# Optimization experiments

Measured on AMD Instinct MI355X. Metric: run time of the kernel, lower is better.

Reference implementation:

```python
import jax, jax.numpy as jnp
import numpy as np

N_FEATURES = 64
D_MODEL = 256


def setup_inputs() -> dict:
    key = jax.random.key(0)
    ks = jax.random.split(key, 6)
    B = 4096
    x = jax.random.normal(ks[0], (B, N_FEATURES), dtype=jnp.float32)
    # Stacked per-feature weights (equivalent to n_features separate MLPs).
    # Linear(1, d): weight [d, 1] -> stacked as [F, d]; bias [F, d]
    s1 = 1.0  # kaiming-uniform-ish scale for fan_in=1
    W1 = jax.random.uniform(ks[1], (N_FEATURES, D_MODEL), jnp.float32, -s1, s1)
    b1 = jax.random.uniform(ks[2], (N_FEATURES, D_MODEL), jnp.float32, -s1, s1)
    # Linear(d, d): weight [d, d] per feature -> [F, d, d]
    s2 = 1.0 / np.sqrt(D_MODEL)
    W2 = jax.random.uniform(ks[3], (N_FEATURES, D_MODEL, D_MODEL), jnp.float32, -s2, s2)
    b2 = jax.random.uniform(ks[4], (N_FEATURES, D_MODEL), jnp.float32, -s2, s2)
    cls_token = jax.random.normal(ks[5], (1, 1, D_MODEL), dtype=jnp.float32)
    return {"x": x, "W1": W1, "b1": b1, "W2": W2, "b2": b2, "cls_token": cls_token}


def reference(x, W1, b1, W2, b2, cls_token):
    # h[b,f,d] = relu(x[b,f] * W1[f,d] + b1[f,d])   (Linear(1,d) per feature)
    h = jax.nn.relu(x[:, :, None] * W1[None, :, :] + b1[None, :, :])
    # out[b,f,e] = h[b,f,:] @ W2[f,:,:] + b2[f,:]   (Linear(d,d) per feature)
    out = jnp.einsum("bfd,fde->bfe", h, W2) + b2[None, :, :]
    cls = jnp.broadcast_to(cls_token, (x.shape[0], 1, out.shape[-1]))
    return jnp.concatenate([cls, out], axis=1)  # [B, F+1, d_model]
```

## Files before the change

kernel.cpp:

```cpp
#include <hip/hip_runtime.h>
#include <hip/hip_bf16.h>


#define B_  4096
#define F_  64
#define D_  256
#define ORS (65 * 256)

using f32x4  = __attribute__((ext_vector_type(4))) float;
using s16x8  = __attribute__((ext_vector_type(8))) short;
typedef unsigned int u32;

__device__ __forceinline__ unsigned short to_bf16_bits(float v) {
    __hip_bfloat16 h = __float2bfloat16(v);
    return *reinterpret_cast<unsigned short*>(&h);
}

__device__ __forceinline__ void gload_lds16(const void* g, void* l) {
    __builtin_amdgcn_global_load_lds(
        (const __attribute__((address_space(1))) u32*)g,
        (__attribute__((address_space(3))) u32*)l, 16, 0, 0);
}

__global__ __launch_bounds__(256) void femb_prep(
    const float* __restrict__ W2, unsigned short* __restrict__ W2s)
{
    const int blk = blockIdx.x;
    const int f   = blk >> 2;
    const int kb  = blk & 3;
    const int t   = threadIdx.x;

    const float* col = W2 + (size_t)f * D_ * D_ + (size_t)(kb * 64) * D_ + t;
    float r[64];
    #pragma unroll
    for (int j = 0; j < 64; ++j) r[j] = col[(size_t)j * D_];

    unsigned short* ob = W2s + (size_t)blk * 16384 + t * 64;
    #pragma unroll
    for (int j8 = 0; j8 < 8; ++j8) {
        union { s16x8 s; unsigned short u[8]; } pk;
        #pragma unroll
        for (int e = 0; e < 8; ++e) pk.u[e] = to_bf16_bits(r[j8 * 8 + e]);
        *reinterpret_cast<s16x8*>(ob + ((j8 ^ (t & 7)) * 8)) = pk.s;
    }
}

__global__ __launch_bounds__(256, 2) void femb_main5(
    const float* __restrict__ x,  const float* __restrict__ W1,
    const float* __restrict__ b1, const unsigned short* __restrict__ W2s,
    const float* __restrict__ b2, const float* __restrict__ cls,
    float* __restrict__ out)
{
    __shared__ float w1s[D_];
    __shared__ float b1s[D_];
    __shared__ float xs[128];
    __shared__ __align__(16) char arena[65536];
    unsigned short* bW0 = (unsigned short*)arena;
    unsigned short* bW1 = (unsigned short*)(arena + 32768);
    float* eb0 = (float*)arena;
    float* eb1 = (float*)(arena + 16640);

    const int tid  = threadIdx.x;
    const int bid  = blockIdx.x;
    const int f    = bid & 63;
    const int row0 = (bid >> 6) << 7;

    w1s[tid] = W1[f * D_ + tid];
    b1s[tid] = b1[f * D_ + tid];
    if (tid < 128) xs[tid] = x[(size_t)(row0 + tid) * F_ + f];

    const int lane = tid & 63;
    const int wid  = tid >> 6;
    const int wm   = wid >> 1;
    const int wn   = wid & 1;
    const int llo  = lane & 15;
    const int lhi  = lane >> 4;

    const char* gsrc = (const char*)(W2s + (size_t)f * 65536);
    f32x4 clsv = *reinterpret_cast<const f32x4*>(cls + lane * 4);

#define STAGE(DST, KB)                                                         \
    {                                                                          \
        const char* gt = gsrc + (KB) * 32768;                                  \
        _Pragma("unroll")                                                      \
        for (int r = 0; r < 8; ++r)                                            \
            gload_lds16(gt + tid * 16 + r * 4096,                              \
                        (char*)(DST) + tid * 16 + r * 4096);                   \
    }

    STAGE(bW0, 0);
    __syncthreads();

    float xv[4];
    #pragma unroll
    for (int mt = 0; mt < 4; ++mt) xv[mt] = xs[wm * 64 + mt * 16 + llo];

    f32x4 acc[4][8];
    #pragma unroll
    for (int mt = 0; mt < 4; ++mt)
        #pragma unroll
        for (int nt = 0; nt < 8; ++nt)
            acc[mt][nt] = (f32x4){0.f, 0.f, 0.f, 0.f};

    #pragma unroll
    for (int kb = 0; kb < 4; ++kb) {
        unsigned short* cur = (kb & 1) ? bW1 : bW0;
        unsigned short* nxt = (kb & 1) ? bW0 : bW1;
        if (kb < 3) STAGE(nxt, kb + 1);

        #pragma unroll
        for (int ks = 0; ks < 2; ++ks) {
            const int kg = kb * 64 + ks * 32 + lhi * 8;
            float w1r[8], b1r[8];
            #pragma unroll
            for (int e = 0; e < 8; ++e) { w1r[e] = w1s[kg + e]; b1r[e] = b1s[kg + e]; }

            s16x8 afrag[4];
            #pragma unroll
            for (int mt = 0; mt < 4; ++mt) {
                union { s16x8 s; unsigned short u[8]; } pk;
                #pragma unroll
                for (int e = 0; e < 8; ++e) {
                    float h = fmaf(xv[mt], w1r[e], b1r[e]);
                    pk.u[e] = to_bf16_bits(fmaxf(h, 0.f));
                }
                afrag[mt] = pk.s;
            }

            const int base16 = (wn * 128 + llo) * 64 + (((ks * 4 + lhi) ^ (llo & 7)) * 8);
            #pragma unroll
            for (int nt = 0; nt < 8; ++nt) {
                s16x8 bfrag = *reinterpret_cast<const s16x8*>(&cur[base16 + nt * 1024]);
                #pragma unroll
                for (int mt = 0; mt < 4; ++mt)
                    acc[mt][nt] = __builtin_amdgcn_mfma_f32_16x16x32_bf16(
                        bfrag, afrag[mt], acc[mt][nt], 0, 0, 0);
            }
        }
        __syncthreads();
    }

    f32x4 b2v = *reinterpret_cast<const f32x4*>(&b2[f * D_ + lane * 4]);

#define EPI_WRITE(C, EB)                                                       \
    if (wm == ((C) >> 2)) {                                                    \
        const int mt_ = (C) & 3;                                               \
        _Pragma("unroll")                                                      \
        for (int nt = 0; nt < 8; ++nt)                                         \
            *reinterpret_cast<f32x4*>(                                         \
                &(EB)[llo * 260 + wn * 128 + nt * 16 + lhi * 4]) = acc[mt_][nt]; \
    }

#define EPI_BAR()                                                              \
    do {                                                                       \
        asm volatile("s_waitcnt lgkmcnt(0)" ::: "memory");                     \
        __builtin_amdgcn_s_barrier();                                          \
        asm volatile("" ::: "memory");                                         \
    } while (0)

#define EPI_READ(C, EB)                                                        \
    {                                                                          \
        _Pragma("unroll")                                                      \
        for (int i = 0; i < 4; ++i) {                                          \
            const int lr = wid * 4 + i;                                        \
            const size_t grow = (size_t)(row0 + (C) * 16 + lr);                \
            f32x4 v = *reinterpret_cast<const f32x4*>(                         \
                          &(EB)[lr * 260 + lane * 4]) + b2v;                   \
            *reinterpret_cast<f32x4*>(out + grow * ORS + (f + 1) * D_ + lane * 4) = v; \
            if (f == 0)                                                        \
                *reinterpret_cast<f32x4*>(out + grow * ORS + lane * 4) = clsv; \
        }                                                                      \
    }

    EPI_WRITE(0, eb0);
    EPI_BAR();
    #pragma unroll
    for (int c = 0; c < 8; ++c) {
        float* curb = (c & 1) ? eb1 : eb0;
        float* nxtb = (c & 1) ? eb0 : eb1;
        if (c < 7) EPI_WRITE(c + 1, nxtb);
        EPI_READ(c, curb);
        if (c < 7) EPI_BAR();
    }
#undef STAGE
#undef EPI_WRITE
#undef EPI_BAR
#undef EPI_READ
}

__global__ void femb_cls(const float* __restrict__ cls, float* __restrict__ out)
{
    int i = blockIdx.x * 256 + threadIdx.x;
    int b = i >> 6;
    int q = i & 63;
    f32x4 v = *reinterpret_cast<const f32x4*>(cls + q * 4);
    *reinterpret_cast<f32x4*>(out + (size_t)b * ORS + q * 4) = v;
}

__global__ __launch_bounds__(256, 2) void femb_main_fb(
    const float* __restrict__ x,  const float* __restrict__ W1,
    const float* __restrict__ b1, const float* __restrict__ W2,
    const float* __restrict__ b2, float* __restrict__ out)
{
    __shared__ float w1s[D_];
    __shared__ float b1s[D_];
    __shared__ float xs[128];
    __shared__ __align__(16) unsigned short bW[256][72];

    const int tid  = threadIdx.x;
    const int bid  = blockIdx.x;
    const int f    = bid & 63;
    const int row0 = (bid >> 6) << 7;

    w1s[tid] = W1[f * D_ + tid];
    b1s[tid] = b1[f * D_ + tid];
    if (tid < 128) xs[tid] = x[(size_t)(row0 + tid) * F_ + f];

    const int lane = tid & 63;
    const int wid  = tid >> 6;
    const int wm   = wid >> 1;
    const int wn   = wid & 1;
    const int llo  = lane & 15;
    const int lhi  = lane >> 4;

    __syncthreads();

    float xv[4];
    #pragma unroll
    for (int mt = 0; mt < 4; ++mt) xv[mt] = xs[wm * 64 + mt * 16 + llo];

    f32x4 acc[4][8];
    #pragma unroll
    for (int mt = 0; mt < 4; ++mt)
        #pragma unroll
        for (int nt = 0; nt < 8; ++nt)
            acc[mt][nt] = (f32x4){0.f, 0.f, 0.f, 0.f};

    const float* w2col = W2 + (size_t)f * D_ * D_ + tid;

    for (int kb = 0; kb < 4; ++kb) {
        float r[64];
        const float* p = w2col + (size_t)(kb * 64) * D_;
        #pragma unroll
        for (int j = 0; j < 64; ++j) r[j] = p[(size_t)j * D_];

        __syncthreads();
        #pragma unroll
        for (int j8 = 0; j8 < 8; ++j8) {
            union { s16x8 s; unsigned short u[8]; } pk;
            #pragma unroll
            for (int e = 0; e < 8; ++e) pk.u[e] = to_bf16_bits(r[j8 * 8 + e]);
            *reinterpret_cast<s16x8*>(&bW[tid][j8 * 8]) = pk.s;
        }
        __syncthreads();

        #pragma unroll
        for (int ks = 0; ks < 2; ++ks) {
            const int kg = kb * 64 + ks * 32 + lhi * 8;
            float w1r[8], b1r[8];
            #pragma unroll
            for (int e = 0; e < 8; ++e) { w1r[e] = w1s[kg + e]; b1r[e] = b1s[kg + e]; }

            s16x8 afrag[4];
            #pragma unroll
            for (int mt = 0; mt < 4; ++mt) {
                union { s16x8 s; unsigned short u[8]; } pk;
                #pragma unroll
                for (int e = 0; e < 8; ++e) {
                    float h = fmaf(xv[mt], w1r[e], b1r[e]);
                    pk.u[e] = to_bf16_bits(fmaxf(h, 0.f));
                }
                afrag[mt] = pk.s;
            }

            const int kl = ks * 32 + lhi * 8;
            #pragma unroll
            for (int nt = 0; nt < 8; ++nt) {
                s16x8 bfrag = *reinterpret_cast<const s16x8*>(
                    &bW[wn * 128 + nt * 16 + llo][kl]);
                #pragma unroll
                for (int mt = 0; mt < 4; ++mt)
                    acc[mt][nt] = __builtin_amdgcn_mfma_f32_16x16x32_bf16(
                        bfrag, afrag[mt], acc[mt][nt], 0, 0, 0);
            }
        }
    }

    const float* b2f = b2 + f * D_;
    float* obase = out + (size_t)(row0 + wm * 64 + llo) * ORS
                       + (f + 1) * D_ + wn * 128 + lhi * 4;
    #pragma unroll
    for (int nt = 0; nt < 8; ++nt) {
        f32x4 bv = *reinterpret_cast<const f32x4*>(&b2f[wn * 128 + nt * 16 + lhi * 4]);
        #pragma unroll
        for (int mt = 0; mt < 4; ++mt) {
            f32x4 v = acc[mt][nt] + bv;
            *reinterpret_cast<f32x4*>(obase + (size_t)mt * 16 * ORS + nt * 16) = v;
        }
    }
}

extern "C" void kernel_launch(void* const* d_in, const int* in_sizes, int n_in,
                              void* d_out, int out_size, void* d_ws, size_t ws_size,
                              hipStream_t stream)
{
    const float* x   = (const float*)d_in[0];
    const float* W1  = (const float*)d_in[1];
    const float* b1  = (const float*)d_in[2];
    const float* W2  = (const float*)d_in[3];
    const float* b2  = (const float*)d_in[4];
    const float* cls = (const float*)d_in[5];
    float* out = (float*)d_out;

    const size_t need = (size_t)F_ * D_ * D_ * sizeof(unsigned short);
    if (ws_size >= need) {
        unsigned short* W2s = (unsigned short*)d_ws;
        femb_prep<<<F_ * 4, 256, 0, stream>>>(W2, W2s);
        femb_main5<<<F_ * (B_ / 128), 256, 0, stream>>>(x, W1, b1, W2s, b2, cls, out);
    } else {
        femb_cls<<<(B_ * 64) / 256, 256, 0, stream>>>(cls, out);
        femb_main_fb<<<F_ * (B_ / 128), 256, 0, stream>>>(x, W1, b1, W2, b2, out);
    }
}
```

Baseline: 78.28 us.

## Shrink LDS staging to 32-wide K slices to fit three blocks per CU

The prep kernel now lays out W2 in bf16 as 32-element K slices with a 4-way XOR swizzle. The main kernel double-buffers 16KB slices over 8 steps instead of 32KB over 4, and uses a smaller epilogue buffer of 8 rows. Together these cut LDS use so launch bounds can request 3 blocks per CU. The feature-to-block mapping is also permuted so concurrently running blocks touch different features. In exchange there are twice as many pipeline barriers and epilogue rounds, and register pressure rises under the tighter occupancy bound.

```diff
diff --git a/kernel.cpp b/kernel.cpp
--- a/kernel.cpp
+++ b/kernel.cpp
@@ -35,17 +35,19 @@
     #pragma unroll
     for (int j = 0; j < 64; ++j) r[j] = col[(size_t)j * D_];
 
-    unsigned short* ob = W2s + (size_t)blk * 16384 + t * 64;
+    unsigned short* ob = W2s + (size_t)blk * 16384;
     #pragma unroll
     for (int j8 = 0; j8 < 8; ++j8) {
         union { s16x8 s; unsigned short u[8]; } pk;
         #pragma unroll
         for (int e = 0; e < 8; ++e) pk.u[e] = to_bf16_bits(r[j8 * 8 + e]);
-        *reinterpret_cast<s16x8*>(ob + ((j8 ^ (t & 7)) * 8)) = pk.s;
-    }
-}
-
-__global__ __launch_bounds__(256, 2) void femb_main5(
+        const int h  = j8 >> 2;
+        const int pp = (j8 & 3) ^ ((t >> 1) & 3);
+        *reinterpret_cast<s16x8*>(ob + h * 8192 + t * 32 + pp * 8) = pk.s;
+    }
+}
+
+__global__ __launch_bounds__(256, 3) void femb_main6(
     const float* __restrict__ x,  const float* __restrict__ W1,
     const float* __restrict__ b1, const unsigned short* __restrict__ W2s,
     const float* __restrict__ b2, const float* __restrict__ cls,
@@ -54,15 +56,12 @@
     __shared__ float w1s[D_];
     __shared__ float b1s[D_];
     __shared__ float xs[128];
-    __shared__ __align__(16) char arena[65536];
-    unsigned short* bW0 = (unsigned short*)arena;
-    unsigned short* bW1 = (unsigned short*)(arena + 32768);
-    float* eb0 = (float*)arena;
-    float* eb1 = (float*)(arena + 16640);
+    __shared__ __align__(16) unsigned short bW[2][8192];
+    __shared__ __align__(16) float eb[2][8 * 260];
 
     const int tid  = threadIdx.x;
     const int bid  = blockIdx.x;
-    const int f    = bid & 63;
+    const int f    = (bid & 7) * 8 + ((bid >> 3) & 7);
     const int row0 = (bid >> 6) << 7;
 
     w1s[tid] = W1[f * D_ + tid];
@@ -76,19 +75,20 @@
     const int llo  = lane & 15;
     const int lhi  = lane >> 4;
 
-    const char* gsrc = (const char*)(W2s + (size_t)f * 65536);
+    const char* gsrc = (const char*)W2s + (size_t)f * 131072;
     f32x4 clsv = *reinterpret_cast<const f32x4*>(cls + lane * 4);
-
-#define STAGE(DST, KB)                                                         \
+    f32x4 b2v  = *reinterpret_cast<const f32x4*>(&b2[f * D_ + lane * 4]);
+
+#define STAGE(DST, S)                                                          \
     {                                                                          \
-        const char* gt = gsrc + (KB) * 32768;                                  \
+        const char* gt = gsrc + (S) * 16384;                                   \
         _Pragma("unroll")                                                      \
-        for (int r = 0; r < 8; ++r)                                            \
+        for (int r = 0; r < 4; ++r)                                            \
             gload_lds16(gt + tid * 16 + r * 4096,                              \
                         (char*)(DST) + tid * 16 + r * 4096);                   \
     }
 
-    STAGE(bW0, 0);
+    STAGE(bW[0], 0);
     __syncthreads();
 
     float xv[4];
@@ -102,11 +102,154 @@
         for (int nt = 0; nt < 8; ++nt)
             acc[mt][nt] = (f32x4){0.f, 0.f, 0.f, 0.f};
 
-    #pragma unroll
+    const int bbase = (wn * 128 + llo) * 32 + ((lhi ^ ((llo >> 1) & 3)) * 8);
+
+    #pragma unroll
+    for (int s = 0; s < 8; ++s) {
+        const unsigned short* cur = bW[s & 1];
+        if (s < 7) STAGE(bW[(s & 1) ^ 1], s + 1);
+
+        const int kg = s * 32 + lhi * 8;
+        float w1r[8], b1r[8];
+        #pragma unroll
+        for (int e = 0; e < 8; ++e) { w1r[e] = w1s[kg + e]; b1r[e] = b1s[kg + e]; }
+
+        s16x8 afrag[4];
+        #pragma unroll
+        for (int mt = 0; mt < 4; ++mt) {
+            union { s16x8 sv; unsigned short u[8]; } pk;
+            #pragma unroll
+            for (int e = 0; e < 8; ++e) {
+                float h = fmaf(xv[mt], w1r[e], b1r[e]);
+                pk.u[e] = to_bf16_bits(fmaxf(h, 0.f));
+            }
+            afrag[mt] = pk.sv;
+        }
+
+        #pragma unroll
+        for (int nt = 0; nt < 8; ++nt) {
+            s16x8 bfrag = *reinterpret_cast<const s16x8*>(&cur[bbase + nt * 512]);
+            #pragma unroll
+            for (int mt = 0; mt < 4; ++mt)
+                acc[mt][nt] = __builtin_amdgcn_mfma_f32_16x16x32_bf16(
+                    bfrag, afrag[mt], acc[mt][nt], 0, 0, 0);
+        }
+        __syncthreads();
+    }
+
+
+#define EPI_WRITE(C, EB)                                                       \
+    if (wm == ((C) >> 3) && ((llo >> 3) == ((C) & 1))) {                       \
+        const int mt_ = ((C) >> 1) & 3;                                        \
+        const int lr_ = llo & 7;                                               \
+        _Pragma("unroll")                                                      \
+        for (int nt = 0; nt < 8; ++nt)                                         \
+            *reinterpret_cast<f32x4*>(                                         \
+                &(EB)[lr_ * 260 + wn * 128 + nt * 16 + lhi * 4]) = acc[mt_][nt]; \
+    }
+
+#define EPI_BAR()                                                              \
+    do {                                                                       \
+        asm volatile("s_waitcnt lgkmcnt(0)" ::: "memory");                     \
+        __builtin_amdgcn_s_barrier();                                          \
+        asm volatile("" ::: "memory");                                         \
+    } while (0)
+
+#define EPI_READ(C, EB)                                                        \
+    {                                                                          \
+        _Pragma("unroll")                                                      \
+        for (int i = 0; i < 2; ++i) {                                          \
+            const int lr_ = wid * 2 + i;                                       \
+            const size_t grow = (size_t)(row0 + (C) * 8 + lr_);                \
+            f32x4 v = *reinterpret_cast<const f32x4*>(                         \
+                          &(EB)[lr_ * 260 + lane * 4]) + b2v;                  \
+            *reinterpret_cast<f32x4*>(out + grow * ORS + (f + 1) * D_ + lane * 4) = v; \
+            if (f == 0)                                                        \
+                *reinterpret_cast<f32x4*>(out + grow * ORS + lane * 4) = clsv; \
+        }                                                                      \
+    }
+
+    EPI_WRITE(0, eb[0]);
+    EPI_BAR();
+    #pragma unroll
+    for (int c = 0; c < 16; ++c) {
+        float* curb = eb[c & 1];
+        float* nxtb = eb[(c & 1) ^ 1];
+        if (c < 15) EPI_WRITE(c + 1, nxtb);
+        EPI_READ(c, curb);
+        if (c < 15) EPI_BAR();
+    }
+#undef STAGE
+#undef EPI_WRITE
+#undef EPI_BAR
+#undef EPI_READ
+}
+
+__global__ void femb_cls(const float* __restrict__ cls, float* __restrict__ out)
+{
+    int i = blockIdx.x * 256 + threadIdx.x;
+    int b = i >> 6;
+    int q = i & 63;
+    f32x4 v = *reinterpret_cast<const f32x4*>(cls + q * 4);
+    *reinterpret_cast<f32x4*>(out + (size_t)b * ORS + q * 4) = v;
+}
+
+__global__ __launch_bounds__(256, 2) void femb_main_fb(
+    const float* __restrict__ x,  const float* __restrict__ W1,
+    const float* __restrict__ b1, const float* __restrict__ W2,
+    const float* __restrict__ b2, float* __restrict__ out)
+{
+    __shared__ float w1s[D_];
+    __shared__ float b1s[D_];
+    __shared__ float xs[128];
+    __shared__ __align__(16) unsigned short bW[256][72];
+
+    const int tid  = threadIdx.x;
+    const int bid  = blockIdx.x;
+    const int f    = bid & 63;
+    const int row0 = (bid >> 6) << 7;
+
+    w1s[tid] = W1[f * D_ + tid];
+    b1s[tid] = b1[f * D_ + tid];
+    if (tid < 128) xs[tid] = x[(size_t)(row0 + tid) * F_ + f];
+
+    const int lane = tid & 63;
+    const int wid  = tid >> 6;
+    const int wm   = wid >> 1;
+    const int wn   = wid & 1;
+    const int llo  = lane & 15;
+    const int lhi  = lane >> 4;
+
+    __syncthreads();
+
+    float xv[4];
+    #pragma unroll
+    for (int mt = 0; mt < 4; ++mt) xv[mt] = xs[wm * 64 + mt * 16 + llo];
+
+    f32x4 acc[4][8];
+    #pragma unroll
+    for (int mt = 0; mt < 4; ++mt)
+        #pragma unroll
+        for (int nt = 0; nt < 8; ++nt)
+            acc[mt][nt] = (f32x4){0.f, 0.f, 0.f, 0.f};
+
+    const float* w2col = W2 + (size_t)f * D_ * D_ + tid;
+
     for (int kb = 0; kb < 4; ++kb) {
-        unsigned short* cur = (kb & 1) ? bW1 : bW0;
-        unsigned short* nxt = (kb & 1) ? bW0 : bW1;
-        if (kb < 3) STAGE(nxt, kb + 1);
+        float r[64];
+        const float* p = w2col + (size_t)(kb * 64) * D_;
+        #pragma unroll
+        for (int j = 0; j < 64; ++j) r[j] = p[(size_t)j * D_];
+
+        __syncthreads();
+        #pragma unroll
+        for (int j8 = 0; j8 < 8; ++j8) {
+            union { s16x8 s; unsigned short u[8]; } pk;
+            #pragma unroll
+            for (int e = 0; e < 8; ++e) pk.u[e] = to_bf16_bits(r[j8 * 8 + e]);
+            *reinterpret_cast<s16x8*>(&bW[tid][j8 * 8]) = pk.s;
+        }
+        __syncthreads();
 
         #pragma unroll
         for (int ks = 0; ks < 2; ++ks) {
@@ -127,152 +270,6 @@
                 afrag[mt] = pk.s;
             }
 
-            const int base16 = (wn * 128 + llo) * 64 + (((ks * 4 + lhi) ^ (llo & 7)) * 8);
-            #pragma unroll
-            for (int nt = 0; nt < 8; ++nt) {
-                s16x8 bfrag = *reinterpret_cast<const s16x8*>(&cur[base16 + nt * 1024]);
-                #pragma unroll
-                for (int mt = 0; mt < 4; ++mt)
-                    acc[mt][nt] = __builtin_amdgcn_mfma_f32_16x16x32_bf16(
-                        bfrag, afrag[mt], acc[mt][nt], 0, 0, 0);
-            }
-        }
-        __syncthreads();
-    }
-
-    f32x4 b2v = *reinterpret_cast<const f32x4*>(&b2[f * D_ + lane * 4]);
-
-#define EPI_WRITE(C, EB)                                                       \
-    if (wm == ((C) >> 2)) {                                                    \
-        const int mt_ = (C) & 3;                                               \
-        _Pragma("unroll")                                                      \
-        for (int nt = 0; nt < 8; ++nt)                                         \
-            *reinterpret_cast<f32x4*>(                                         \
-                &(EB)[llo * 260 + wn * 128 + nt * 16 + lhi * 4]) = acc[mt_][nt]; \
-    }
-
-#define EPI_BAR()                                                              \
-    do {                                                                       \
-        asm volatile("s_waitcnt lgkmcnt(0)" ::: "memory");                     \
-        __builtin_amdgcn_s_barrier();                                          \
-        asm volatile("" ::: "memory");                                         \
-    } while (0)
-
-#define EPI_READ(C, EB)                                                        \
-    {                                                                          \
-        _Pragma("unroll")                                                      \
-        for (int i = 0; i < 4; ++i) {                                          \
-            const int lr = wid * 4 + i;                                        \
-            const size_t grow = (size_t)(row0 + (C) * 16 + lr);                \
-            f32x4 v = *reinterpret_cast<const f32x4*>(                         \
-                          &(EB)[lr * 260 + lane * 4]) + b2v;                   \
-            *reinterpret_cast<f32x4*>(out + grow * ORS + (f + 1) * D_ + lane * 4) = v; \
-            if (f == 0)                                                        \
-                *reinterpret_cast<f32x4*>(out + grow * ORS + lane * 4) = clsv; \
-        }                                                                      \
-    }
-
-    EPI_WRITE(0, eb0);
-    EPI_BAR();
-    #pragma unroll
-    for (int c = 0; c < 8; ++c) {
-        float* curb = (c & 1) ? eb1 : eb0;
-        float* nxtb = (c & 1) ? eb0 : eb1;
-        if (c < 7) EPI_WRITE(c + 1, nxtb);
-        EPI_READ(c, curb);
-        if (c < 7) EPI_BAR();
-    }
-#undef STAGE
-#undef EPI_WRITE
-#undef EPI_BAR
-#undef EPI_READ
-}
-
-__global__ void femb_cls(const float* __restrict__ cls, float* __restrict__ out)
-{
-    int i = blockIdx.x * 256 + threadIdx.x;
-    int b = i >> 6;
-    int q = i & 63;
-    f32x4 v = *reinterpret_cast<const f32x4*>(cls + q * 4);
-    *reinterpret_cast<f32x4*>(out + (size_t)b * ORS + q * 4) = v;
-}
-
-__global__ __launch_bounds__(256, 2) void femb_main_fb(
-    const float* __restrict__ x,  const float* __restrict__ W1,
-    const float* __restrict__ b1, const float* __restrict__ W2,
-    const float* __restrict__ b2, float* __restrict__ out)
-{
-    __shared__ float w1s[D_];
-    __shared__ float b1s[D_];
-    __shared__ float xs[128];
-    __shared__ __align__(16) unsigned short bW[256][72];
-
-    const int tid  = threadIdx.x;
-    const int bid  = blockIdx.x;
-    const int f    = bid & 63;
-    const int row0 = (bid >> 6) << 7;
-
-    w1s[tid] = W1[f * D_ + tid];
-    b1s[tid] = b1[f * D_ + tid];
-    if (tid < 128) xs[tid] = x[(size_t)(row0 + tid) * F_ + f];
-
-    const int lane = tid & 63;
-    const int wid  = tid >> 6;
-    const int wm   = wid >> 1;
-    const int wn   = wid & 1;
-    const int llo  = lane & 15;
-    const int lhi  = lane >> 4;
-
-    __syncthreads();
-
-    float xv[4];
-    #pragma unroll
-    for (int mt = 0; mt < 4; ++mt) xv[mt] = xs[wm * 64 + mt * 16 + llo];
-
-    f32x4 acc[4][8];
-    #pragma unroll
-    for (int mt = 0; mt < 4; ++mt)
-        #pragma unroll
-        for (int nt = 0; nt < 8; ++nt)
-            acc[mt][nt] = (f32x4){0.f, 0.f, 0.f, 0.f};
-
-    const float* w2col = W2 + (size_t)f * D_ * D_ + tid;
-
-    for (int kb = 0; kb < 4; ++kb) {
-        float r[64];
-        const float* p = w2col + (size_t)(kb * 64) * D_;
-        #pragma unroll
-        for (int j = 0; j < 64; ++j) r[j] = p[(size_t)j * D_];
-
-        __syncthreads();
-        #pragma unroll
-        for (int j8 = 0; j8 < 8; ++j8) {
-            union { s16x8 s; unsigned short u[8]; } pk;
-            #pragma unroll
-            for (int e = 0; e < 8; ++e) pk.u[e] = to_bf16_bits(r[j8 * 8 + e]);
-            *reinterpret_cast<s16x8*>(&bW[tid][j8 * 8]) = pk.s;
-        }
-        __syncthreads();
-
-        #pragma unroll
-        for (int ks = 0; ks < 2; ++ks) {
-            const int kg = kb * 64 + ks * 32 + lhi * 8;
-            float w1r[8], b1r[8];
-            #pragma unroll
-            for (int e = 0; e < 8; ++e) { w1r[e] = w1s[kg + e]; b1r[e] = b1s[kg + e]; }
-
-            s16x8 afrag[4];
-            #pragma unroll
-            for (int mt = 0; mt < 4; ++mt) {
-                union { s16x8 s; unsigned short u[8]; } pk;
-                #pragma unroll
-                for (int e = 0; e < 8; ++e) {
-                    float h = fmaf(xv[mt], w1r[e], b1r[e]);
-                    pk.u[e] = to_bf16_bits(fmaxf(h, 0.f));
-                }
-                afrag[mt] = pk.s;
-            }
-
             const int kl = ks * 32 + lhi * 8;
             #pragma unroll
             for (int nt = 0; nt < 8; ++nt) {
@@ -316,7 +313,7 @@
     if (ws_size >= need) {
         unsigned short* W2s = (unsigned short*)d_ws;
         femb_prep<<<F_ * 4, 256, 0, stream>>>(W2, W2s);
-        femb_main5<<<F_ * (B_ / 128), 256, 0, stream>>>(x, W1, b1, W2s, b2, cls, out);
+        femb_main6<<<F_ * (B_ / 128), 256, 0, stream>>>(x, W1, b1, W2s, b2, cls, out);
     } else {
         femb_cls<<<(B_ * 64) / 256, 256, 0, stream>>>(cls, out);
         femb_main_fb<<<F_ * (B_ / 128), 256, 0, stream>>>(x, W1, b1, W2, b2, out);
```

After: 104.0 us. 1.33x slower.
